# Performance work log

Measured on AMD Instinct MI355X. Metric: run time of the kernel, lower is better.

The kernel has to match this reference:

```python
import jax, jax.numpy as jnp
import numpy as np

N_NODES = 50000
N_EDGES = 800000
D_IN = 128
D_HID = 128
NUM_LAYERS = 3
NUM_GRAPHS = 50


def setup_inputs() -> dict:
    key = jax.random.key(0)
    ks = jax.random.split(key, 8)
    x = jax.random.normal(ks[0], (N_NODES, D_IN), dtype=jnp.float32)
    edge_index = jax.random.randint(ks[1], (2, N_EDGES), 0, N_NODES, dtype=jnp.int32)
    batch = jnp.sort(jax.random.randint(ks[2], (N_NODES,), 0, NUM_GRAPHS, dtype=jnp.int32))
    # glorot-ish init for GCN weights and fc weights
    scale = 1.0 / np.sqrt(D_HID)
    Wc = jax.random.normal(ks[3], (NUM_LAYERS, D_IN, D_HID), dtype=jnp.float32) * scale
    bc = jnp.zeros((NUM_LAYERS, D_HID), dtype=jnp.float32)
    Wf = jax.random.normal(ks[4], (NUM_LAYERS, D_HID, D_HID), dtype=jnp.float32) * scale
    bf = jnp.zeros((NUM_LAYERS, D_HID), dtype=jnp.float32)
    return {"x": x, "edge_index": edge_index, "batch": batch,
            "Wc": Wc, "bc": bc, "Wf": Wf, "bf": bf}


def _gcn_forward(x, Wc, bc, Wf, bf, src, dst, deg_inv_sqrt, batch):
    norm = deg_inv_sqrt[src] * deg_inv_sqrt[dst]  # [E+N]
    for i in range(NUM_LAYERS):
        h = x @ Wc[i]                              # [N, D_HID] linear transform
        msg = h[src] * norm[:, None]               # gather + normalize, [E+N, D_HID]
        x = jax.ops.segment_sum(msg, dst, num_segments=N_NODES) + bc[i]
        x = jax.nn.relu(x)
    x = jax.ops.segment_sum(x, batch, num_segments=NUM_GRAPHS)  # global_add_pool
    for i in range(NUM_LAYERS):
        x = jax.nn.relu(x @ Wf[i] + bf[i])
    return x  # [NUM_GRAPHS, D_HID]


def reference(x, edge_index, batch, Wc, bc, Wf, bf):
    # add self-loops (PyG GCNConv default) and compute symmetric normalization
    loops = jnp.arange(N_NODES, dtype=edge_index.dtype)
    src = jnp.concatenate([edge_index[0], loops])
    dst = jnp.concatenate([edge_index[1], loops])
    deg = jax.ops.segment_sum(jnp.ones_like(dst, dtype=x.dtype), dst,
                              num_segments=N_NODES)
    deg_inv_sqrt = jnp.where(deg > 0, jax.lax.rsqrt(jnp.maximum(deg, 1.0)), 0.0)
    return _gcn_forward(x, Wc, bc, Wf, bf, src, dst, deg_inv_sqrt, batch)
```

## Files before the change

kernel.cpp:

```cpp
#include <hip/hip_runtime.h>

#define N_NODES 50000
#define N_EDGES 800000
#define D 128
#define NGRAPH 50

typedef unsigned int uint32;
typedef unsigned short u16;
typedef __attribute__((ext_vector_type(8))) short short8;
typedef __attribute__((ext_vector_type(4))) float f32x4;

__device__ inline float bf_lo(uint32 u) { union { uint32 u; float f; } c; c.u = u << 16; return c.f; }
__device__ inline float bf_hi(uint32 u) { union { uint32 u; float f; } c; c.u = u & 0xffff0000u; return c.f; }
__device__ inline u16 f2bf(float f) {
  union { float f; uint32 u; } c; c.f = f;
  uint32 r = (c.u + 0x7fffu + ((c.u >> 16) & 1u)) >> 16;
  return (u16)r;
}

__global__ void k_init(int* __restrict__ deg, const float* __restrict__ Wc,
                       u16* __restrict__ WT, const int* __restrict__ batch,
                       int* __restrict__ gstart) {
  int i = blockIdx.x * 256 + threadIdx.x;
  if (i < N_NODES) deg[i] = 0;
  if (i < 3 * 128 * 128) {
    int layer = i >> 14, rem = i & 16383;
    int n = rem >> 7, k = rem & 127;
    WT[i] = f2bf(Wc[layer * 16384 + k * 128 + n]);
  }
  if (i <= NGRAPH) {
    int lo = 0, hi = N_NODES;
    while (lo < hi) {
      int mid = (lo + hi) >> 1;
      if (batch[mid] < i) lo = mid + 1; else hi = mid;
    }
    gstart[i] = lo;
  }
}

__global__ void k_degfill(const int* __restrict__ src, const int* __restrict__ dst,
                          int* __restrict__ deg, u16* __restrict__ csr) {
  int part = blockIdx.x & 7;
  int e = (blockIdx.x >> 3) * 256 + threadIdx.x;
  if (e < N_EDGES) {
    int d = dst[e];
    if (d / 6250 == part) {
      int r = atomicAdd(&deg[d], 1);
      csr[(d << 6) + r] = (u16)src[e];
    }
  }
}

template <int AF32>
__global__ __launch_bounds__(256) void k_gemm(const void* __restrict__ Ap,
                                              const u16* __restrict__ WT,
                                              const int* __restrict__ deg,
                                              u16* __restrict__ G) {
  __shared__ u16 so[4][16][136];
  int t = threadIdx.x;
  int wave = t >> 6, l = t & 63;
  int cl = l & 15, kgrp = l >> 4;
  int r0 = blockIdx.x * 64 + wave * 16;
  int arow = r0 + cl;
  bool valid = arow < N_NODES;

  const short8* B8 = reinterpret_cast<const short8*>(WT);

  f32x4 acc[8] = {};
#pragma unroll
  for (int k0 = 0; k0 < 4; ++k0) {
    short8 a = {};
    if (valid) {
      if (AF32) {
        const float4* A4 = reinterpret_cast<const float4*>(Ap);
        float4 v0 = A4[(size_t)arow * 32 + (k0 * 4 + kgrp) * 2];
        float4 v1 = A4[(size_t)arow * 32 + (k0 * 4 + kgrp) * 2 + 1];
        a[0] = (short)f2bf(v0.x); a[1] = (short)f2bf(v0.y);
        a[2] = (short)f2bf(v0.z); a[3] = (short)f2bf(v0.w);
        a[4] = (short)f2bf(v1.x); a[5] = (short)f2bf(v1.y);
        a[6] = (short)f2bf(v1.z); a[7] = (short)f2bf(v1.w);
      } else {
        a = reinterpret_cast<const short8*>(Ap)[(size_t)arow * 16 + k0 * 4 + kgrp];
      }
    }
#pragma unroll
    for (int c = 0; c < 8; ++c) {
      short8 b = B8[(c * 16 + cl) * 16 + k0 * 4 + kgrp];
      acc[c] = __builtin_amdgcn_mfma_f32_16x16x32_bf16(a, b, acc[c], 0, 0, 0);
    }
  }

  int rloc = kgrp * 4;
  float dj[4];
#pragma unroll
  for (int j = 0; j < 4; ++j) {
    int rr = r0 + rloc + j;
    dj[j] = (rr < N_NODES) ? rsqrtf((float)deg[rr] + 1.0f) : 0.f;
  }
#pragma unroll
  for (int c = 0; c < 8; ++c) {
#pragma unroll
    for (int j = 0; j < 4; ++j) {
      so[wave][rloc + j][c * 16 + cl] = f2bf(dj[j] * acc[c][j]);
    }
  }
#pragma unroll
  for (int i = 0; i < 4; ++i) {
    int idx = i * 64 + l;
    int rr = idx >> 4, ch = idx & 15;
    int grow = r0 + rr;
    if (grow < N_NODES) {
      *reinterpret_cast<uint4*>(&(((u16*)G)[(size_t)grow * 128 + ch * 8])) =
          *reinterpret_cast<const uint4*>(&so[wave][rr][ch * 8]);
    }
  }
}

#define ACC8(A, u) do { \
    A##0 += bf_lo((u).x); A##1 += bf_hi((u).x); A##2 += bf_lo((u).y); A##3 += bf_hi((u).y); \
    A##4 += bf_lo((u).z); A##5 += bf_hi((u).z); A##6 += bf_lo((u).w); A##7 += bf_hi((u).w); } while (0)

#define RED2(v) do { v += __shfl_xor(v, 16); v += __shfl_xor(v, 32); } while (0)

__global__ __launch_bounds__(256) void k_agg(const uint4* __restrict__ g4,
                                             const int* __restrict__ deg,
                                             const u16* __restrict__ csr,
                                             const float* __restrict__ bc,
                                             uint4* __restrict__ xo) {
  int w = threadIdx.x >> 6;
  int i0 = blockIdx.x * 8 + w * 2;
  if (i0 >= N_NODES) return;
  int i1 = i0 + 1;
  bool has1 = i1 < N_NODES;
  int l = threadIdx.x & 63;
  int q = l >> 4, c = l & 15;

  int cntA = deg[i0];
  int cntB = has1 ? deg[i1] : 0;
  float diA = rsqrtf((float)cntA + 1.0f);
  float diB = rsqrtf((float)cntB + 1.0f);

  float xA0 = 0.f, xA1 = 0.f, xA2 = 0.f, xA3 = 0.f, xA4 = 0.f, xA5 = 0.f, xA6 = 0.f, xA7 = 0.f;
  float xB0 = 0.f, xB1 = 0.f, xB2 = 0.f, xB3 = 0.f, xB4 = 0.f, xB5 = 0.f, xB6 = 0.f, xB7 = 0.f;

  if (q == 0) {
    uint4 su = g4[(size_t)i0 * 16 + c];
    ACC8(xA, su);
  } else if (q == 1 && has1) {
    uint4 su = g4[(size_t)i1 * 16 + c];
    ACC8(xB, su);
  }

  int myA = (l < cntA) ? (int)csr[(i0 << 6) + l] : 0;
  int myB = (l < cntB && has1) ? (int)csr[(i1 << 6) + l] : 0;

  int nq = (max(cntA, cntB) + 3) >> 2;
#pragma unroll 4
  for (int j = 0; j < nq; ++j) {
    int idx = 4 * j + q;
    int sA = __shfl(myA, idx < cntA ? idx : 0);
    int sB = __shfl(myB, idx < cntB ? idx : 0);
    uint4 uA = g4[(size_t)sA * 16 + c];
    uint4 uB = g4[(size_t)sB * 16 + c];
    if (idx < cntA) ACC8(xA, uA);
    if (idx < cntB) ACC8(xB, uB);
  }

  RED2(xA0); RED2(xA1); RED2(xA2); RED2(xA3); RED2(xA4); RED2(xA5); RED2(xA6); RED2(xA7);
  RED2(xB0); RED2(xB1); RED2(xB2); RED2(xB3); RED2(xB4); RED2(xB5); RED2(xB6); RED2(xB7);

  int node = (q == 0) ? i0 : i1;
  if (q < 2 && (q == 0 || has1)) {
    float di = (q == 0) ? diA : diB;
    float r0 = (q == 0) ? xA0 : xB0, r1 = (q == 0) ? xA1 : xB1;
    float r2 = (q == 0) ? xA2 : xB2, r3 = (q == 0) ? xA3 : xB3;
    float r4 = (q == 0) ? xA4 : xB4, r5 = (q == 0) ? xA5 : xB5;
    float r6 = (q == 0) ? xA6 : xB6, r7 = (q == 0) ? xA7 : xB7;
    float4 b0 = reinterpret_cast<const float4*>(bc)[c * 2];
    float4 b1 = reinterpret_cast<const float4*>(bc)[c * 2 + 1];
    r0 = fmaxf(fmaf(di, r0, b0.x), 0.f);
    r1 = fmaxf(fmaf(di, r1, b0.y), 0.f);
    r2 = fmaxf(fmaf(di, r2, b0.z), 0.f);
    r3 = fmaxf(fmaf(di, r3, b0.w), 0.f);
    r4 = fmaxf(fmaf(di, r4, b1.x), 0.f);
    r5 = fmaxf(fmaf(di, r5, b1.y), 0.f);
    r6 = fmaxf(fmaf(di, r6, b1.z), 0.f);
    r7 = fmaxf(fmaf(di, r7, b1.w), 0.f);
    uint4 o;
    o.x = ((uint32)f2bf(r1) << 16) | f2bf(r0);
    o.y = ((uint32)f2bf(r3) << 16) | f2bf(r2);
    o.z = ((uint32)f2bf(r5) << 16) | f2bf(r4);
    o.w = ((uint32)f2bf(r7) << 16) | f2bf(r6);
    xo[(size_t)node * 16 + c] = o;
  }
}

__global__ __launch_bounds__(256) void k_pool(const uint32* __restrict__ xb,
                                              const int* __restrict__ gstart,
                                              float* __restrict__ pp) {
  __shared__ float2 red[4][64];
  int g = blockIdx.x, ch = blockIdx.y;
  int s = gstart[g], e = gstart[g + 1];
  long len = e - s;
  int cs = s + (int)(len * ch / 8);
  int ce = s + (int)(len * (ch + 1) / 8);
  int sub = threadIdx.x >> 6, l = threadIdx.x & 63;
  float2 acc = make_float2(0.f, 0.f);
  for (int n = cs + sub; n < ce; n += 4) {
    uint32 v = xb[(size_t)n * 64 + l];
    acc.x += bf_lo(v);
    acc.y += bf_hi(v);
  }
  red[sub][l] = acc;
  __syncthreads();
  if (sub == 0) {
    float2 a = red[0][l];
    a.x += red[1][l].x + red[2][l].x + red[3][l].x;
    a.y += red[1][l].y + red[2][l].y + red[3][l].y;
    pp[(ch * NGRAPH + g) * D + 2 * l] = a.x;
    pp[(ch * NGRAPH + g) * D + 2 * l + 1] = a.y;
  }
}

__global__ __launch_bounds__(128) void k_fc(const float* __restrict__ pp,
                                            const float* __restrict__ Wf,
                                            const float* __restrict__ bf,
                                            float* __restrict__ out) {
  __shared__ float row[D];
  int g = blockIdx.x, c = threadIdx.x;
  float v = 0.f;
#pragma unroll
  for (int ch = 0; ch < 8; ++ch) v += pp[(ch * NGRAPH + g) * D + c];
  row[c] = v;
  __syncthreads();
  for (int l = 0; l < 3; ++l) {
    const float* W = Wf + l * D * D;
    float s = bf[l * D + c];
    for (int k = 0; k < D; ++k) s = fmaf(row[k], W[k * D + c], s);
    s = fmaxf(s, 0.f);
    __syncthreads();
    row[c] = s;
    __syncthreads();
  }
  out[g * D + c] = row[c];
}

extern "C" void kernel_launch(void* const* d_in, const int* in_sizes, int n_in,
                              void* d_out, int out_size, void* d_ws, size_t ws_size,
                              hipStream_t stream) {
  const float* x   = (const float*)d_in[0];
  const int*   ei  = (const int*)d_in[1];
  const int* batch = (const int*)d_in[2];
  const float* Wc  = (const float*)d_in[3];
  const float* bc  = (const float*)d_in[4];
  const float* Wf  = (const float*)d_in[5];
  const float* bf  = (const float*)d_in[6];
  float* out = (float*)d_out;
  const int* src = ei;
  const int* dst = ei + N_EDGES;

  char* ws = (char*)d_ws;
  size_t o = 0;
  auto take = [&](size_t b) -> void* {
    void* p = ws + o;
    o = (o + b + 255) & ~(size_t)255;
    return p;
  };
  int*  deg    = (int*)take(N_NODES * 4);
  int*  gstart = (int*)take(64 * 4);
  u16*  WT     = (u16*)take((size_t)3 * D * D * 2);
  u16*  csr    = (u16*)take((size_t)N_NODES * 64 * 2);
  u16*  xb     = (u16*)take((size_t)N_NODES * D * 2);
  u16*  gbuf   = (u16*)take((size_t)N_NODES * D * 2);
  float* pp    = (float*)take((size_t)8 * NGRAPH * D * 4);
  (void)ws_size; (void)in_sizes; (void)n_in; (void)out_size;

  const int NB = (N_NODES + 255) / 256;
  k_init<<<NB, 256, 0, stream>>>(deg, Wc, WT, batch, gstart);
  k_degfill<<<8 * ((N_EDGES + 255) / 256), 256, 0, stream>>>(src, dst, deg, csr);

  const int GB = (N_NODES + 63) / 64;
  const int AB = (N_NODES + 7) / 8;
  k_gemm<1><<<GB, 256, 0, stream>>>(x, WT + 0 * D * D, deg, gbuf);
  k_agg<<<AB, 256, 0, stream>>>((const uint4*)gbuf, deg, csr, bc + 0 * D, (uint4*)xb);
  k_gemm<0><<<GB, 256, 0, stream>>>(xb, WT + 1 * D * D, deg, gbuf);
  k_agg<<<AB, 256, 0, stream>>>((const uint4*)gbuf, deg, csr, bc + 1 * D, (uint4*)xb);
  k_gemm<0><<<GB, 256, 0, stream>>>(xb, WT + 2 * D * D, deg, gbuf);
  k_agg<<<AB, 256, 0, stream>>>((const uint4*)gbuf, deg, csr, bc + 2 * D, (uint4*)xb);

  k_pool<<<dim3(NGRAPH, 8), 256, 0, stream>>>((const uint32*)xb, gstart, pp);
  k_fc<<<NGRAPH, 128, 0, stream>>>(pp, Wf, bf, out);
}
```

Before: 233.4 us.

## Fuse aggregation and GEMM per layer using aggregate-then-transform reordering

Reorders each GCN layer to aggregate the degree-prescaled input features first and then apply the weight matrix, which lets one kernel do gather, MFMA GEMM, bias, ReLU and the next layer's prescale. A new prescale kernel converts x to bf16 scaled by deg^-1/2. This removes the separate GEMM kernels and the intermediate gbuf round trip through global memory. The cost is that each wave now processes 16 nodes serially in the gather phase with less parallelism per block, so latency hiding in the irregular gather may drop, and bf16 rounding now happens before the transform.

After: 232.5 us. Within noise of the previous version (-0.4%).

```diff
diff --git a/kernel.cpp b/kernel.cpp
--- a/kernel.cpp
+++ b/kernel.cpp
@@ -51,46 +51,107 @@
   }
 }
 
-template <int AF32>
-__global__ __launch_bounds__(256) void k_gemm(const void* __restrict__ Ap,
-                                              const u16* __restrict__ WT,
-                                              const int* __restrict__ deg,
-                                              u16* __restrict__ G) {
-  __shared__ u16 so[4][16][136];
+__global__ void k_prescale(const float4* __restrict__ x, const int* __restrict__ deg,
+                           uint4* __restrict__ xs) {
+  int i = blockIdx.x * 256 + threadIdx.x;
+  if (i < N_NODES * 16) {
+    int node = i >> 4;
+    float di = rsqrtf((float)deg[node] + 1.0f);
+    float4 v0 = x[(size_t)i * 2];
+    float4 v1 = x[(size_t)i * 2 + 1];
+    uint4 o;
+    o.x = ((uint32)f2bf(di * v0.y) << 16) | f2bf(di * v0.x);
+    o.y = ((uint32)f2bf(di * v0.w) << 16) | f2bf(di * v0.z);
+    o.z = ((uint32)f2bf(di * v1.y) << 16) | f2bf(di * v1.x);
+    o.w = ((uint32)f2bf(di * v1.w) << 16) | f2bf(di * v1.z);
+    xs[i] = o;
+  }
+}
+
+#define ACC8(A, u) do { \
+    A##0 += bf_lo((u).x); A##1 += bf_hi((u).x); A##2 += bf_lo((u).y); A##3 += bf_hi((u).y); \
+    A##4 += bf_lo((u).z); A##5 += bf_hi((u).z); A##6 += bf_lo((u).w); A##7 += bf_hi((u).w); } while (0)
+
+#define RED2(v) do { v += __shfl_xor(v, 16); v += __shfl_xor(v, 32); } while (0)
+
+template <int PRESCALE_OUT>
+__global__ __launch_bounds__(256) void k_layer(const uint4* __restrict__ xs,
+                                               const int* __restrict__ deg,
+                                               const u16* __restrict__ csr,
+                                               const u16* __restrict__ WT,
+                                               const float* __restrict__ bc,
+                                               u16* __restrict__ xo) {
+  __shared__ u16 sa[4][16][136];
   int t = threadIdx.x;
   int wave = t >> 6, l = t & 63;
-  int cl = l & 15, kgrp = l >> 4;
+  int q = l >> 4, c = l & 15;
   int r0 = blockIdx.x * 64 + wave * 16;
-  int arow = r0 + cl;
-  bool valid = arow < N_NODES;
+
+  for (int n = 0; n < 16; n += 2) {
+    int i0 = r0 + n, i1 = i0 + 1;
+    bool v0 = i0 < N_NODES, v1 = i1 < N_NODES;
+    int cntA = v0 ? deg[i0] : 0;
+    int cntB = v1 ? deg[i1] : 0;
+
+    float xA0 = 0.f, xA1 = 0.f, xA2 = 0.f, xA3 = 0.f, xA4 = 0.f, xA5 = 0.f, xA6 = 0.f, xA7 = 0.f;
+    float xB0 = 0.f, xB1 = 0.f, xB2 = 0.f, xB3 = 0.f, xB4 = 0.f, xB5 = 0.f, xB6 = 0.f, xB7 = 0.f;
+
+    if (q == 0 && v0) {
+      uint4 su = xs[(size_t)i0 * 16 + c];
+      ACC8(xA, su);
+    } else if (q == 1 && v1) {
+      uint4 su = xs[(size_t)i1 * 16 + c];
+      ACC8(xB, su);
+    }
+
+    int myA = (l < cntA) ? (int)csr[(i0 << 6) + l] : 0;
+    int myB = (l < cntB) ? (int)csr[(i1 << 6) + l] : 0;
+
+    int nq = (max(cntA, cntB) + 3) >> 2;
+#pragma unroll 4
+    for (int j = 0; j < nq; ++j) {
+      int idx = 4 * j + q;
+      int sA = __shfl(myA, idx < cntA ? idx : 0);
+      int sB = __shfl(myB, idx < cntB ? idx : 0);
+      uint4 uA = xs[(size_t)sA * 16 + c];
+      uint4 uB = xs[(size_t)sB * 16 + c];
+      if (idx < cntA) ACC8(xA, uA);
+      if (idx < cntB) ACC8(xB, uB);
+    }
+
+    RED2(xA0); RED2(xA1); RED2(xA2); RED2(xA3); RED2(xA4); RED2(xA5); RED2(xA6); RED2(xA7);
+    RED2(xB0); RED2(xB1); RED2(xB2); RED2(xB3); RED2(xB4); RED2(xB5); RED2(xB6); RED2(xB7);
+
+    if (q == 0) {
+      uint4 o;
+      o.x = ((uint32)f2bf(xA1) << 16) | f2bf(xA0);
+      o.y = ((uint32)f2bf(xA3) << 16) | f2bf(xA2);
+      o.z = ((uint32)f2bf(xA5) << 16) | f2bf(xA4);
+      o.w = ((uint32)f2bf(xA7) << 16) | f2bf(xA6);
+      *reinterpret_cast<uint4*>(&sa[wave][n][c * 8]) = o;
+    } else if (q == 1) {
+      uint4 o;
+      o.x = ((uint32)f2bf(xB1) << 16) | f2bf(xB0);
+      o.y = ((uint32)f2bf(xB3) << 16) | f2bf(xB2);
+      o.z = ((uint32)f2bf(xB5) << 16) | f2bf(xB4);
+      o.w = ((uint32)f2bf(xB7) << 16) | f2bf(xB6);
+      *reinterpret_cast<uint4*>(&sa[wave][n + 1][c * 8]) = o;
+    }
+  }
 
   const short8* B8 = reinterpret_cast<const short8*>(WT);
-
   f32x4 acc[8] = {};
 #pragma unroll
   for (int k0 = 0; k0 < 4; ++k0) {
-    short8 a = {};
-    if (valid) {
-      if (AF32) {
-        const float4* A4 = reinterpret_cast<const float4*>(Ap);
-        float4 v0 = A4[(size_t)arow * 32 + (k0 * 4 + kgrp) * 2];
-        float4 v1 = A4[(size_t)arow * 32 + (k0 * 4 + kgrp) * 2 + 1];
-        a[0] = (short)f2bf(v0.x); a[1] = (short)f2bf(v0.y);
-        a[2] = (short)f2bf(v0.z); a[3] = (short)f2bf(v0.w);
-        a[4] = (short)f2bf(v1.x); a[5] = (short)f2bf(v1.y);
-        a[6] = (short)f2bf(v1.z); a[7] = (short)f2bf(v1.w);
-      } else {
-        a = reinterpret_cast<const short8*>(Ap)[(size_t)arow * 16 + k0 * 4 + kgrp];
-      }
-    }
-#pragma unroll
-    for (int c = 0; c < 8; ++c) {
-      short8 b = B8[(c * 16 + cl) * 16 + k0 * 4 + kgrp];
-      acc[c] = __builtin_amdgcn_mfma_f32_16x16x32_bf16(a, b, acc[c], 0, 0, 0);
-    }
-  }
-
-  int rloc = kgrp * 4;
+    short8 a = *reinterpret_cast<const short8*>(&sa[wave][c][(k0 * 4 + q) * 8]);
+#pragma unroll
+    for (int cc = 0; cc < 8; ++cc) {
+      short8 b = B8[(cc * 16 + c) * 16 + k0 * 4 + q];
+      acc[cc] = __builtin_amdgcn_mfma_f32_16x16x32_bf16(a, b, acc[cc], 0, 0, 0);
+    }
+  }
+
+  int rloc = q * 4;
   float dj[4];
 #pragma unroll
   for (int j = 0; j < 4; ++j) {
@@ -98,100 +159,25 @@
     dj[j] = (rr < N_NODES) ? rsqrtf((float)deg[rr] + 1.0f) : 0.f;
   }
 #pragma unroll
-  for (int c = 0; c < 8; ++c) {
+  for (int cc = 0; cc < 8; ++cc) {
+    float bcv = bc[cc * 16 + c];
 #pragma unroll
     for (int j = 0; j < 4; ++j) {
-      so[wave][rloc + j][c * 16 + cl] = f2bf(dj[j] * acc[c][j]);
-    }
-  }
+      float r = fmaxf(fmaf(dj[j], acc[cc][j], bcv), 0.f);
+      if (PRESCALE_OUT) r *= dj[j];
+      sa[wave][rloc + j][cc * 16 + c] = f2bf(r);
+    }
+  }
+
 #pragma unroll
   for (int i = 0; i < 4; ++i) {
     int idx = i * 64 + l;
     int rr = idx >> 4, ch = idx & 15;
     int grow = r0 + rr;
     if (grow < N_NODES) {
-      *reinterpret_cast<uint4*>(&(((u16*)G)[(size_t)grow * 128 + ch * 8])) =
-          *reinterpret_cast<const uint4*>(&so[wave][rr][ch * 8]);
-    }
-  }
-}
-
-#define ACC8(A, u) do { \
-    A##0 += bf_lo((u).x); A##1 += bf_hi((u).x); A##2 += bf_lo((u).y); A##3 += bf_hi((u).y); \
-    A##4 += bf_lo((u).z); A##5 += bf_hi((u).z); A##6 += bf_lo((u).w); A##7 += bf_hi((u).w); } while (0)
-
-#define RED2(v) do { v += __shfl_xor(v, 16); v += __shfl_xor(v, 32); } while (0)
-
-__global__ __launch_bounds__(256) void k_agg(const uint4* __restrict__ g4,
-                                             const int* __restrict__ deg,
-                                             const u16* __restrict__ csr,
-                                             const float* __restrict__ bc,
-                                             uint4* __restrict__ xo) {
-  int w = threadIdx.x >> 6;
-  int i0 = blockIdx.x * 8 + w * 2;
-  if (i0 >= N_NODES) return;
-  int i1 = i0 + 1;
-  bool has1 = i1 < N_NODES;
-  int l = threadIdx.x & 63;
-  int q = l >> 4, c = l & 15;
-
-  int cntA = deg[i0];
-  int cntB = has1 ? deg[i1] : 0;
-  float diA = rsqrtf((float)cntA + 1.0f);
-  float diB = rsqrtf((float)cntB + 1.0f);
-
-  float xA0 = 0.f, xA1 = 0.f, xA2 = 0.f, xA3 = 0.f, xA4 = 0.f, xA5 = 0.f, xA6 = 0.f, xA7 = 0.f;
-  float xB0 = 0.f, xB1 = 0.f, xB2 = 0.f, xB3 = 0.f, xB4 = 0.f, xB5 = 0.f, xB6 = 0.f, xB7 = 0.f;
-
-  if (q == 0) {
-    uint4 su = g4[(size_t)i0 * 16 + c];
-    ACC8(xA, su);
-  } else if (q == 1 && has1) {
-    uint4 su = g4[(size_t)i1 * 16 + c];
-    ACC8(xB, su);
-  }
-
-  int myA = (l < cntA) ? (int)csr[(i0 << 6) + l] : 0;
-  int myB = (l < cntB && has1) ? (int)csr[(i1 << 6) + l] : 0;
-
-  int nq = (max(cntA, cntB) + 3) >> 2;
-#pragma unroll 4
-  for (int j = 0; j < nq; ++j) {
-    int idx = 4 * j + q;
-    int sA = __shfl(myA, idx < cntA ? idx : 0);
-    int sB = __shfl(myB, idx < cntB ? idx : 0);
-    uint4 uA = g4[(size_t)sA * 16 + c];
-    uint4 uB = g4[(size_t)sB * 16 + c];
-    if (idx < cntA) ACC8(xA, uA);
-    if (idx < cntB) ACC8(xB, uB);
-  }
-
-  RED2(xA0); RED2(xA1); RED2(xA2); RED2(xA3); RED2(xA4); RED2(xA5); RED2(xA6); RED2(xA7);
-  RED2(xB0); RED2(xB1); RED2(xB2); RED2(xB3); RED2(xB4); RED2(xB5); RED2(xB6); RED2(xB7);
-
-  int node = (q == 0) ? i0 : i1;
-  if (q < 2 && (q == 0 || has1)) {
-    float di = (q == 0) ? diA : diB;
-    float r0 = (q == 0) ? xA0 : xB0, r1 = (q == 0) ? xA1 : xB1;
-    float r2 = (q == 0) ? xA2 : xB2, r3 = (q == 0) ? xA3 : xB3;
-    float r4 = (q == 0) ? xA4 : xB4, r5 = (q == 0) ? xA5 : xB5;
-    float r6 = (q == 0) ? xA6 : xB6, r7 = (q == 0) ? xA7 : xB7;
-    float4 b0 = reinterpret_cast<const float4*>(bc)[c * 2];
-    float4 b1 = reinterpret_cast<const float4*>(bc)[c * 2 + 1];
-    r0 = fmaxf(fmaf(di, r0, b0.x), 0.f);
-    r1 = fmaxf(fmaf(di, r1, b0.y), 0.f);
-    r2 = fmaxf(fmaf(di, r2, b0.z), 0.f);
-    r3 = fmaxf(fmaf(di, r3, b0.w), 0.f);
-    r4 = fmaxf(fmaf(di, r4, b1.x), 0.f);
-    r5 = fmaxf(fmaf(di, r5, b1.y), 0.f);
-    r6 = fmaxf(fmaf(di, r6, b1.z), 0.f);
-    r7 = fmaxf(fmaf(di, r7, b1.w), 0.f);
-    uint4 o;
-    o.x = ((uint32)f2bf(r1) << 16) | f2bf(r0);
-    o.y = ((uint32)f2bf(r3) << 16) | f2bf(r2);
-    o.z = ((uint32)f2bf(r5) << 16) | f2bf(r4);
-    o.w = ((uint32)f2bf(r7) << 16) | f2bf(r6);
-    xo[(size_t)node * 16 + c] = o;
+      *reinterpret_cast<uint4*>(&xo[(size_t)grow * 128 + ch * 8]) =
+          *reinterpret_cast<const uint4*>(&sa[wave][rr][ch * 8]);
+    }
   }
 }
 
@@ -270,24 +256,21 @@
   int*  gstart = (int*)take(64 * 4);
   u16*  WT     = (u16*)take((size_t)3 * D * D * 2);
   u16*  csr    = (u16*)take((size_t)N_NODES * 64 * 2);
-  u16*  xb     = (u16*)take((size_t)N_NODES * D * 2);
-  u16*  gbuf   = (u16*)take((size_t)N_NODES * D * 2);
+  u16*  xsA    = (u16*)take((size_t)N_NODES * D * 2);
+  u16*  xsB    = (u16*)take((size_t)N_NODES * D * 2);
   float* pp    = (float*)take((size_t)8 * NGRAPH * D * 4);
   (void)ws_size; (void)in_sizes; (void)n_in; (void)out_size;
 
   const int NB = (N_NODES + 255) / 256;
   k_init<<<NB, 256, 0, stream>>>(deg, Wc, WT, batch, gstart);
   k_degfill<<<8 * ((N_EDGES + 255) / 256), 256, 0, stream>>>(src, dst, deg, csr);
+  k_prescale<<<(N_NODES * 16 + 255) / 256, 256, 0, stream>>>((const float4*)x, deg, (uint4*)xsA);
 
   const int GB = (N_NODES + 63) / 64;
-  const int AB = (N_NODES + 7) / 8;
-  k_gemm<1><<<GB, 256, 0, stream>>>(x, WT + 0 * D * D, deg, gbuf);
-  k_agg<<<AB, 256, 0, stream>>>((const uint4*)gbuf, deg, csr, bc + 0 * D, (uint4*)xb);
-  k_gemm<0><<<GB, 256, 0, stream>>>(xb, WT + 1 * D * D, deg, gbuf);
-  k_agg<<<AB, 256, 0, stream>>>((const uint4*)gbuf, deg, csr, bc + 1 * D, (uint4*)xb);
-  k_gemm<0><<<GB, 256, 0, stream>>>(xb, WT + 2 * D * D, deg, gbuf);
-  k_agg<<<AB, 256, 0, stream>>>((const uint4*)gbuf, deg, csr, bc + 2 * D, (uint4*)xb);
-
-  k_pool<<<dim3(NGRAPH, 8), 256, 0, stream>>>((const uint32*)xb, gstart, pp);
+  k_layer<1><<<GB, 256, 0, stream>>>((const uint4*)xsA, deg, csr, WT + 0 * D * D, bc + 0 * D, xsB);
+  k_layer<1><<<GB, 256, 0, stream>>>((const uint4*)xsB, deg, csr, WT + 1 * D * D, bc + 1 * D, xsA);
+  k_layer<0><<<GB, 256, 0, stream>>>((const uint4*)xsA, deg, csr, WT + 2 * D * D, bc + 2 * D, xsB);
+
+  k_pool<<<dim3(NGRAPH, 8), 256, 0, stream>>>((const uint32*)xsB, gstart, pp);
   k_fc<<<NGRAPH, 128, 0, stream>>>(pp, Wf, bf, out);
 }
```
